# Kernel tuning notes

Hardware: AMD Instinct MI355X
Metric: run time of the kernel (lower is better)

Reference implementation:

```python
import jax, jax.numpy as jnp
import numpy as np

ATT_DIM = 1024
N_HEADS = 16
D_HEAD = ATT_DIM // N_HEADS
LARGE = 1e30  # fp32 masking constant used by masked_softmax


def setup_inputs() -> dict:
    key = jax.random.key(0)
    ks = jax.random.split(key, 12)
    B, Tq, Tv, D = 4, 2048, 2048, 1024
    s = 1.0 / np.sqrt(D)
    sf = 1.0 / np.sqrt(ATT_DIM)
    return {
        "query": jax.random.normal(ks[0], (B, Tq, D), jnp.float32),
        "value": jax.random.normal(ks[1], (B, Tv, D), jnp.float32),
        "value_lens": jax.random.randint(ks[2], (B,), 0, Tv, jnp.int32),
        "Wq": jax.random.normal(ks[3], (D, ATT_DIM), jnp.float32) * s,
        "bq": jnp.zeros((ATT_DIM,), jnp.float32),
        "Wk": jax.random.normal(ks[4], (D, ATT_DIM), jnp.float32) * s,
        "bk": jnp.zeros((ATT_DIM,), jnp.float32),
        "Wv": jax.random.normal(ks[5], (D, ATT_DIM), jnp.float32) * s,
        "bv": jnp.zeros((ATT_DIM,), jnp.float32),
        "Wf": jax.random.normal(ks[6], (ATT_DIM, ATT_DIM), jnp.float32) * sf,
        "bf": jnp.zeros((ATT_DIM,), jnp.float32),
    }


def _attention(query, value, value_lens, Wq, bq, Wk, bk, Wv, bv, Wf, bf):
    B, Tq, _ = query.shape
    Tv = value.shape[1]
    # projections
    k = value @ Wk + bk                     # [B,Tv,att_dim]
    v = value @ Wv + bv                     # [B,Tv,att_dim]
    q = (query @ Wq + bq) / jnp.sqrt(jnp.asarray(D_HEAD, query.dtype))
    # split heads
    q = q.reshape(B, Tq, N_HEADS, D_HEAD)
    k = k.reshape(B, Tv, N_HEADS, D_HEAD)
    v = v.reshape(B, Tv, N_HEADS, D_HEAD)
    # energy: [B, n_heads, Tq, Tv]
    energy = jnp.einsum("bind,bjnd->bnij", q, k)
    # sequence mask: [B,1,1,Tv]
    mask = (jnp.arange(Tv)[None, :] < value_lens[:, None]).astype(energy.dtype)
    energy = energy - (1.0 - mask)[:, None, None, :] * jnp.asarray(LARGE, energy.dtype)
    att_weight = jax.nn.softmax(energy, axis=-1)
    # context: [B, Tq, n_heads, d_head] -> [B, Tq, att_dim]
    context = jnp.einsum("bnij,bjnd->bind", att_weight, v).reshape(B, Tq, ATT_DIM)
    return context @ Wf + bf  # final_att (num_att_head > 1)


def reference(query, value, value_lens, Wq, bq, Wk, bk, Wv, bv, Wf, bf):
    return _attention(query, value, value_lens, Wq, bq, Wk, bk, Wv, bv, Wf, bf)
```

## Files before the change

### kernel.cpp

```cpp
#include <hip/hip_runtime.h>
#include <hip/hip_bf16.h>

typedef __attribute__((ext_vector_type(8))) short short8;
typedef __attribute__((ext_vector_type(4))) float f32x4;
typedef unsigned short u16;
typedef unsigned int u32;
typedef __attribute__((ext_vector_type(8))) unsigned short u16x8;
typedef __attribute__((ext_vector_type(4))) unsigned short u16x4;

__device__ __forceinline__ u16 f2bf(float f) {
    u32 u = __builtin_bit_cast(u32, f);
    u += 0x7FFFu + ((u >> 16) & 1u);
    return (u16)(u >> 16);
}
__device__ __forceinline__ u32 packbf2(float a, float b) {
    return ((u32)f2bf(b) << 16) | (u32)f2bf(a);
}
__device__ __forceinline__ float fexp2(float x) { return exp2f(x); }

__device__ __forceinline__ int swz(int row, int col) {
    return (row * 128 + col * 2) ^ ((row & 7) << 4);
}

__device__ __forceinline__ void gl16(const void* g, void* l) {
    __builtin_amdgcn_global_load_lds(
        (const __attribute__((address_space(1))) unsigned int*)g,
        (__attribute__((address_space(3))) unsigned int*)l, 16, 0, 0);
}

#define FENCE() asm volatile("" ::: "memory")
#define BARRIER() do { FENCE(); __builtin_amdgcn_s_barrier(); FENCE(); } while (0)

__global__ __launch_bounds__(256)
void cvt_kernel(const float* __restrict__ query, const float* __restrict__ value,
                u16* __restrict__ qB, u16* __restrict__ vB)
{
    int bid = blockIdx.x;
    const float* src; u16* dst;
    if (bid < 4096) { src = query; dst = qB; }
    else            { src = value; dst = vB; bid -= 4096; }
    const int i = bid * 256 + threadIdx.x;
    const float4 a = ((const float4*)src)[2 * i];
    const float4 b = ((const float4*)src)[2 * i + 1];
    u16x8 h;
    h[0] = f2bf(a.x); h[1] = f2bf(a.y); h[2] = f2bf(a.z); h[3] = f2bf(a.w);
    h[4] = f2bf(b.x); h[5] = f2bf(b.y); h[6] = f2bf(b.z); h[7] = f2bf(b.w);
    ((u16x8*)dst)[i] = h;
}

__global__ __launch_bounds__(256)
void wtrans_kernel(const float* __restrict__ W0, const float* __restrict__ W1,
                   const float* __restrict__ W2, const float* __restrict__ W3,
                   u16* __restrict__ T0, u16* __restrict__ T1,
                   u16* __restrict__ T2, u16* __restrict__ T3)
{
    const float* W; u16* T;
    switch (blockIdx.z) {
        case 0:  W = W0; T = T0; break;
        case 1:  W = W1; T = T1; break;
        case 2:  W = W2; T = T2; break;
        default: W = W3; T = T3; break;
    }
    __shared__ u16 tile[32][33];
    const int tid = threadIdx.x;
    const int n0 = blockIdx.x * 32, k0 = blockIdx.y * 32;
    const int r = tid >> 3, c = (tid & 7) * 4;
    float4 v = *(const float4*)(W + (size_t)(k0 + r) * 1024 + n0 + c);
    tile[c + 0][r] = f2bf(v.x);
    tile[c + 1][r] = f2bf(v.y);
    tile[c + 2][r] = f2bf(v.z);
    tile[c + 3][r] = f2bf(v.w);
    __syncthreads();
    u16x4 h;
    h[0] = tile[r][c]; h[1] = tile[r][c + 1]; h[2] = tile[r][c + 2]; h[3] = tile[r][c + 3];
    *(u16x4*)(T + (size_t)(n0 + r) * 1024 + k0 + c) = h;
}

#define GNK 32

__device__ __forceinline__ void stage_a(const u16* __restrict__ A, unsigned char* bufA,
                                        int row0, int kt, int tid) {
    const int r = tid >> 2, s = tid & 3;
    gl16((const unsigned char*)A + (size_t)(row0 + r) * 2048 + kt * 64 + ((s ^ (r & 3)) << 4),
         bufA + tid * 16);
}
__device__ __forceinline__ void stage_b(const u16* __restrict__ BT, unsigned char* bufB,
                                        int col0, int kt, int hb, int tid) {
    const int r = hb * 128 + (tid >> 2), s = tid & 3;
    gl16((const unsigned char*)BT + (size_t)(col0 + r) * 2048 + kt * 64 + ((s ^ (r & 3)) << 4),
         bufB + hb * 8192 + tid * 16);
}

__device__ __forceinline__ void gemm_core(const u16* __restrict__ A, const u16* __restrict__ BT,
                                          int row0, int col0, unsigned char* smem,
                                          int tid, int wm, int wn, int l15, int lhi,
                                          f32x4 acc[4][4])
{
    const int slot = (lhi ^ (l15 & 3)) << 4;
    #pragma unroll
    for (int kt = 0; kt < 3; ++kt) {
        unsigned char* buf = smem + kt * 24576;
        stage_a(A, buf, row0, kt, tid);
        stage_b(BT, buf + 8192, col0, kt, 0, tid);
        stage_b(BT, buf + 8192, col0, kt, 1, tid);
    }
    asm volatile("s_waitcnt vmcnt(6)" ::: "memory");
    BARRIER();

    for (int k = 0; k < GNK; ++k) {
        unsigned char* bufA = smem + (k & 3) * 24576;
        unsigned char* bufB = bufA + 8192;
        const bool st = (k + 3 < GNK);
        unsigned char* nbuf = smem + ((k + 3) & 3) * 24576;

        short8 a0, a1, a2, a3, b0, b1;
        a0 = *(const short8*)(bufA + (wm * 64 + 0 * 16 + l15) * 64 + slot);
        a1 = *(const short8*)(bufA + (wm * 64 + 1 * 16 + l15) * 64 + slot);
        a2 = *(const short8*)(bufA + (wm * 64 + 2 * 16 + l15) * 64 + slot);
        a3 = *(const short8*)(bufA + (wm * 64 + 3 * 16 + l15) * 64 + slot);
        b0 = *(const short8*)(bufB + (wn * 64 + 0 * 16 + l15) * 64 + slot);
        b1 = *(const short8*)(bufB + (wn * 64 + 1 * 16 + l15) * 64 + slot);
        if (st) stage_a(A, nbuf, row0, k + 3, tid);
        BARRIER();
        __builtin_amdgcn_s_setprio(1);
        acc[0][0] = __builtin_amdgcn_mfma_f32_16x16x32_bf16(a0, b0, acc[0][0], 0, 0, 0);
        acc[0][1] = __builtin_amdgcn_mfma_f32_16x16x32_bf16(a0, b1, acc[0][1], 0, 0, 0);
        acc[1][0] = __builtin_amdgcn_mfma_f32_16x16x32_bf16(a1, b0, acc[1][0], 0, 0, 0);
        acc[1][1] = __builtin_amdgcn_mfma_f32_16x16x32_bf16(a1, b1, acc[1][1], 0, 0, 0);
        acc[2][0] = __builtin_amdgcn_mfma_f32_16x16x32_bf16(a2, b0, acc[2][0], 0, 0, 0);
        acc[2][1] = __builtin_amdgcn_mfma_f32_16x16x32_bf16(a2, b1, acc[2][1], 0, 0, 0);
        acc[3][0] = __builtin_amdgcn_mfma_f32_16x16x32_bf16(a3, b0, acc[3][0], 0, 0, 0);
        acc[3][1] = __builtin_amdgcn_mfma_f32_16x16x32_bf16(a3, b1, acc[3][1], 0, 0, 0);
        __builtin_amdgcn_s_setprio(0);
        BARRIER();

        short8 b2, b3;
        b2 = *(const short8*)(bufB + (wn * 64 + 2 * 16 + l15) * 64 + slot);
        b3 = *(const short8*)(bufB + (wn * 64 + 3 * 16 + l15) * 64 + slot);
        if (st) {
            stage_b(BT, nbuf + 8192, col0, k + 3, 0, tid);
            stage_b(BT, nbuf + 8192, col0, k + 3, 1, tid);
        }
        if (k < GNK - 3)       asm volatile("s_waitcnt vmcnt(6)" ::: "memory");
        else if (k == GNK - 3) asm volatile("s_waitcnt vmcnt(3)" ::: "memory");
        else if (k == GNK - 2) asm volatile("s_waitcnt vmcnt(0)" ::: "memory");
        BARRIER();
        __builtin_amdgcn_s_setprio(1);
        acc[0][2] = __builtin_amdgcn_mfma_f32_16x16x32_bf16(a0, b2, acc[0][2], 0, 0, 0);
        acc[0][3] = __builtin_amdgcn_mfma_f32_16x16x32_bf16(a0, b3, acc[0][3], 0, 0, 0);
        acc[1][2] = __builtin_amdgcn_mfma_f32_16x16x32_bf16(a1, b2, acc[1][2], 0, 0, 0);
        acc[1][3] = __builtin_amdgcn_mfma_f32_16x16x32_bf16(a1, b3, acc[1][3], 0, 0, 0);
        acc[2][2] = __builtin_amdgcn_mfma_f32_16x16x32_bf16(a2, b2, acc[2][2], 0, 0, 0);
        acc[2][3] = __builtin_amdgcn_mfma_f32_16x16x32_bf16(a2, b3, acc[2][3], 0, 0, 0);
        acc[3][2] = __builtin_amdgcn_mfma_f32_16x16x32_bf16(a3, b2, acc[3][2], 0, 0, 0);
        acc[3][3] = __builtin_amdgcn_mfma_f32_16x16x32_bf16(a3, b3, acc[3][3], 0, 0, 0);
        __builtin_amdgcn_s_setprio(0);
        BARRIER();
    }
}

__global__ __launch_bounds__(512, 2)
void proj_kernel(const u16* __restrict__ queryB, const u16* __restrict__ valueB,
                 const u16* __restrict__ WqT, const u16* __restrict__ WkT,
                 const u16* __restrict__ WvT,
                 const float* __restrict__ bq, const float* __restrict__ bk,
                 const float* __restrict__ bv,
                 u16* __restrict__ Qb, u16* __restrict__ Kb, u16* __restrict__ Vt)
{
    __shared__ __align__(16) unsigned char smem[98304];
    const int t = (blockIdx.x & 7) * 96 + (blockIdx.x >> 3);
    const int z = t >> 8;
    const int tile = t & 255;
    const int row0 = (tile >> 2) * 128, col0 = (tile & 3) * 256;

    const u16* A    = (z == 0) ? queryB : valueB;
    const u16* BT   = (z == 0) ? WqT : (z == 1) ? WkT : WvT;
    const float* bias = (z == 0) ? bq : (z == 1) ? bk : bv;

    const int tid = threadIdx.x;
    const int lane = tid & 63, w = tid >> 6;
    const int wm = w >> 2, wn = w & 3;
    const int l15 = lane & 15, lhi = lane >> 4;

    f32x4 acc[4][4];
    const f32x4 fz = {0.f, 0.f, 0.f, 0.f};
    #pragma unroll
    for (int m = 0; m < 4; ++m)
        #pragma unroll
        for (int n = 0; n < 4; ++n) acc[m][n] = fz;

    gemm_core(A, BT, row0, col0, smem, tid, wm, wn, l15, lhi, acc);

    if (z < 2) {
        u16* out = (z == 0) ? Qb : Kb;
        const float scale = (z == 0) ? 0.18033688011112042f : 1.0f;
        const int bb = row0 >> 11;
        #pragma unroll
        for (int n = 0; n < 4; ++n) {
            int col = col0 + wn * 64 + n * 16 + l15;
            int hh = col >> 6, d = col & 63;
            float bv2 = bias[col];
            #pragma unroll
            for (int m = 0; m < 4; ++m) {
                int rbase = row0 + wm * 64 + m * 16 + lhi * 4;
                #pragma unroll
                for (int rr = 0; rr < 4; ++rr) {
                    int trow = (rbase + rr) & 2047;
                    out[(((size_t)bb * 16 + hh) * 2048 + trow) * 64 + d] =
                        f2bf((acc[m][n][rr] + bv2) * scale);
                }
            }
        }
    } else {
        __syncthreads();
        u16* vl = (u16*)smem;
        #pragma unroll
        for (int n = 0; n < 4; ++n) {
            int c = wn * 64 + n * 16 + l15;
            float bv2 = bias[col0 + c];
            #pragma unroll
            for (int m = 0; m < 4; ++m) {
                int rl = wm * 64 + m * 16 + lhi * 4;
                u16x4 h;
                #pragma unroll
                for (int rr = 0; rr < 4; ++rr) h[rr] = f2bf(acc[m][n][rr] + bv2);
                *(u16x4*)(vl + c * 132 + rl) = h;
            }
        }
        __syncthreads();
        const int bb = row0 >> 11, t0 = row0 & 2047;
        const int c = tid >> 1, hseg = tid & 1;
        const int col = col0 + c;
        const int hh = col >> 6, d = col & 63;
        size_t gb = (((size_t)bb * 16 + hh) * 64 + d) * 2048 + t0 + hseg * 64;
        #pragma unroll
        for (int j = 0; j < 8; ++j) {
            u16x8 v = *(const u16x8*)(vl + c * 132 + hseg * 64 + j * 8);
            *(u16x8*)(Vt + gb + j * 8) = v;
        }
    }
}

__global__ __launch_bounds__(512, 2)
void fgemm_kernel(const u16* __restrict__ Ctx, const u16* __restrict__ WfT,
                  const float* __restrict__ bias, float* __restrict__ out)
{
    __shared__ __align__(16) unsigned char smem[98304];
    const int t = (blockIdx.x & 7) * 32 + (blockIdx.x >> 3);
    const int row0 = (t >> 2) * 128, col0 = (t & 3) * 256;

    const int tid = threadIdx.x;
    const int lane = tid & 63, w = tid >> 6;
    const int wm = w >> 2, wn = w & 3;
    const int l15 = lane & 15, lhi = lane >> 4;

    f32x4 acc[4][4];
    const f32x4 fz = {0.f, 0.f, 0.f, 0.f};
    #pragma unroll
    for (int m = 0; m < 4; ++m)
        #pragma unroll
        for (int n = 0; n < 4; ++n) acc[m][n] = fz;

    gemm_core(Ctx, WfT, row0, col0, smem, tid, wm, wn, l15, lhi, acc);

    #pragma unroll
    for (int n = 0; n < 4; ++n) {
        int col = col0 + wn * 64 + n * 16 + l15;
        float bv2 = bias[col];
        #pragma unroll
        for (int m = 0; m < 4; ++m) {
            int rbase = row0 + wm * 64 + m * 16 + lhi * 4;
            #pragma unroll
            for (int rr = 0; rr < 4; ++rr)
                out[(size_t)(rbase + rr) * 1024 + col] = acc[m][n][rr] + bv2;
        }
    }
}

__global__ __launch_bounds__(512, 4)
void attn_kernel(const u16* __restrict__ Qb, const u16* __restrict__ Kb,
                 const u16* __restrict__ Vt, const int* __restrict__ lens,
                 u16* __restrict__ Ctx)
{
    __shared__ __align__(16) unsigned char ksm[2][8192];
    __shared__ __align__(16) unsigned char vsm[2][8192];

    const int tid = threadIdx.x;
    const int lane = tid & 63;
    const int w = tid >> 6;
    const int l15 = lane & 15, lhi = lane >> 4;
    const int t0id = (blockIdx.x & 7) * 128 + (blockIdx.x >> 3);
    const int qt = t0id & 15;
    const int hid2 = t0id >> 4;
    const int b = hid2 & 3, hh = hid2 >> 2;
    const size_t head = (size_t)(b * 16 + hh);
    const unsigned char* Kbase = (const unsigned char*)Kb + head * (2048 * 128);
    const unsigned char* Vbase = (const unsigned char*)Vt + head * (2048 * 128);
    const unsigned char* Qbase = (const unsigned char*)Qb + head * (2048 * 128) + (size_t)qt * (128 * 128);

    const int o0 = w * 1024 + lane * 16;
    const int r0 = o0 >> 7;
    const int sc0 = (o0 & 127) ^ ((r0 & 7) << 4);

    const int lens_b = lens[b];
    const bool uniform = (lens_b == 0);
    const int len = uniform ? 2048 : lens_b;
    const int nt = (len + 63) >> 6;
    const bool tail = (!uniform) && ((len & 63) != 0);

    auto stage = [&](int t, int bi) {
        gl16(Kbase + (size_t)t * 8192 + (size_t)r0 * 128 + sc0, ksm[bi] + o0);
        gl16(Vbase + (size_t)t * 128 + (size_t)r0 * 4096 + sc0, vsm[bi] + o0);
    };
    stage(0, 0);

    short8 qa[2];
    #pragma unroll
    for (int ks = 0; ks < 2; ++ks)
        qa[ks] = *(const short8*)(Qbase + (w * 16 + l15) * 128 + ks * 64 + lhi * 16);

    __syncthreads();

    float m = -1e30f, lsum = 0.f;
    const f32x4 fz = {0.f, 0.f, 0.f, 0.f};
    f32x4 cT[4];
    #pragma unroll
    for (int nf = 0; nf < 4; ++nf) cT[nf] = fz;

    const int srcA = l15 + (((2 * lhi) & 3) << 4);
    const int srcB = l15 + (((2 * lhi + 1) & 3) << 4);
    const bool hi = lhi >= 2;

    for (int t = 0; t < nt; ++t) {
        const int cur = t & 1;
        if (t + 1 < nt) stage(t + 1, cur ^ 1);

        f32x4 s[4];
        #pragma unroll
        for (int jf = 0; jf < 4; ++jf) s[jf] = fz;
        if (!uniform) {
            __builtin_amdgcn_s_setprio(1);
            #pragma unroll
            for (int ks = 0; ks < 2; ++ks)
                #pragma unroll
                for (int jf = 0; jf < 4; ++jf) {
                    short8 kb = *(const short8*)(ksm[cur] + swz(jf * 16 + l15, ks * 32 + lhi * 8));
                    s[jf] = __builtin_amdgcn_mfma_f32_16x16x32_bf16(kb, qa[ks], s[jf], 0, 0, 0);
                }
            __builtin_amdgcn_s_setprio(0);
            if (tail && t == nt - 1) {
                const int kvb = t * 64 + lhi * 4;
                #pragma unroll
                for (int jf = 0; jf < 4; ++jf)
                    #pragma unroll
                    for (int r = 0; r < 4; ++r)
                        if (kvb + jf * 16 + r >= len) s[jf][r] = -1e30f;
            }
        }
        f32x4 m4;
        #pragma unroll
        for (int r = 0; r < 4; ++r)
            m4[r] = fmaxf(fmaxf(s[0][r], s[1][r]), fmaxf(s[2][r], s[3][r]));
        float tmax = fmaxf(fmaxf(m4[0], m4[1]), fmaxf(m4[2], m4[3]));
        tmax = fmaxf(tmax, __shfl_xor(tmax, 16));
        tmax = fmaxf(tmax, __shfl_xor(tmax, 32));
        const float mnew = fmaxf(m, tmax);
        if (__any(tmax > m)) {
            const float sc = fexp2(m - mnew);
            lsum *= sc;
            #pragma unroll
            for (int nf = 0; nf < 4; ++nf)
                #pragma unroll
                for (int r = 0; r < 4; ++r) cT[nf][r] *= sc;
        }
        m = mnew;
        #pragma unroll
        for (int jf = 0; jf < 4; ++jf)
            #pragma unroll
            for (int r = 0; r < 4; ++r)
                s[jf][r] = fexp2(s[jf][r] - m);
        f32x4 s4;
        #pragma unroll
        for (int r = 0; r < 4; ++r)
            s4[r] = (s[0][r] + s[1][r]) + (s[2][r] + s[3][r]);
        float rs = (s4[0] + s4[1]) + (s4[2] + s4[3]);
        rs += __shfl_xor(rs, 16);
        rs += __shfl_xor(rs, 32);
        lsum += rs;
        u32 pk[4][2];
        #pragma unroll
        for (int jf = 0; jf < 4; ++jf) {
            pk[jf][0] = packbf2(s[jf][0], s[jf][1]);
            pk[jf][1] = packbf2(s[jf][2], s[jf][3]);
        }
        short8 pb[2];
        #pragma unroll
        for (int ks = 0; ks < 2; ++ks) {
            u32 a0, a1, a2, a3;
            { u32 x0 = (u32)__shfl((int)pk[2 * ks][0], srcA); u32 x1 = (u32)__shfl((int)pk[2 * ks + 1][0], srcA); a0 = hi ? x1 : x0; }
            { u32 x0 = (u32)__shfl((int)pk[2 * ks][1], srcA); u32 x1 = (u32)__shfl((int)pk[2 * ks + 1][1], srcA); a1 = hi ? x1 : x0; }
            { u32 x0 = (u32)__shfl((int)pk[2 * ks][0], srcB); u32 x1 = (u32)__shfl((int)pk[2 * ks + 1][0], srcB); a2 = hi ? x1 : x0; }
            { u32 x0 = (u32)__shfl((int)pk[2 * ks][1], srcB); u32 x1 = (u32)__shfl((int)pk[2 * ks + 1][1], srcB); a3 = hi ? x1 : x0; }
            typedef __attribute__((ext_vector_type(4))) unsigned int u32x4_t;
            u32x4_t av = {a0, a1, a2, a3};
            pb[ks] = __builtin_bit_cast(short8, av);
        }
        __builtin_amdgcn_s_setprio(1);
        #pragma unroll
        for (int ks = 0; ks < 2; ++ks)
            #pragma unroll
            for (int nf = 0; nf < 4; ++nf) {
                short8 vb = *(const short8*)(vsm[cur] + swz(nf * 16 + l15, ks * 32 + lhi * 8));
                cT[nf] = __builtin_amdgcn_mfma_f32_16x16x32_bf16(vb, pb[ks], cT[nf], 0, 0, 0);
            }
        __builtin_amdgcn_s_setprio(0);
        __syncthreads();
    }

    const float inv = 1.0f / lsum;
    const int trow = qt * 128 + w * 16 + l15;
    u16* op = Ctx + ((size_t)b * 2048 + trow) * 1024 + hh * 64 + lhi * 4;
    #pragma unroll
    for (int nf = 0; nf < 4; ++nf) {
        u16x4 h;
        #pragma unroll
        for (int r = 0; r < 4; ++r) h[r] = f2bf(cT[nf][r] * inv);
        *(u16x4*)(op + nf * 16) = h;
    }
}

extern "C" void kernel_launch(void* const* d_in, const int* in_sizes, int n_in,
                              void* d_out, int out_size, void* d_ws, size_t ws_size,
                              hipStream_t stream)
{
    (void)in_sizes; (void)n_in; (void)out_size; (void)ws_size;
    const float* query = (const float*)d_in[0];
    const float* value = (const float*)d_in[1];
    const int*   lens  = (const int*)d_in[2];
    const float* Wq = (const float*)d_in[3];
    const float* bq = (const float*)d_in[4];
    const float* Wk = (const float*)d_in[5];
    const float* bk = (const float*)d_in[6];
    const float* Wv = (const float*)d_in[7];
    const float* bv = (const float*)d_in[8];
    const float* Wf = (const float*)d_in[9];
    const float* bfp = (const float*)d_in[10];

    unsigned char* ws = (unsigned char*)d_ws;
    const size_t MB = (size_t)1 << 20;
    u16* WqT = (u16*)(ws + 0 * MB);
    u16* WkT = (u16*)(ws + 2 * MB);
    u16* WvT = (u16*)(ws + 4 * MB);
    u16* WfT = (u16*)(ws + 6 * MB);
    u16* Qb  = (u16*)(ws + 8 * MB);
    u16* Kb  = (u16*)(ws + 24 * MB);
    u16* Vt  = (u16*)(ws + 40 * MB);
    u16* Ctx = (u16*)(ws + 56 * MB);

    u16* queryB = (u16*)d_out;
    u16* valueB = queryB + (size_t)8192 * 1024;

    dim3 tb(256);
    cvt_kernel<<<dim3(8192), tb, 0, stream>>>(query, value, queryB, valueB);
    wtrans_kernel<<<dim3(32, 32, 4), tb, 0, stream>>>(Wq, Wk, Wv, Wf, WqT, WkT, WvT, WfT);

    proj_kernel<<<dim3(768), dim3(512), 0, stream>>>(queryB, valueB, WqT, WkT, WvT,
                                                     bq, bk, bv, Qb, Kb, Vt);

    attn_kernel<<<dim3(1024), dim3(512), 0, stream>>>(Qb, Kb, Vt, lens, Ctx);

    fgemm_kernel<<<dim3(256), dim3(512), 0, stream>>>(Ctx, WfT, bfp, (float*)d_out);
}
```

Baseline: 211.4 us.

## Compute softmax row sums via MFMA with ones, lazy rescale, hardware bf16 pack

The attention kernel drops the per-row sum of exponentials, which used a reduction tree plus cross-lane shuffles, and instead computes it with an extra MFMA that multiplies the bf16 probabilities by a ones vector. The running max is now updated only when the new max exceeds the old one by more than 8 (log2 domain), which skips most rescales of the accumulators. Manual bf16 rounding is replaced with the v_cvt_pk_bf16_f32 instruction. The trade-offs: the denominator is now summed from bf16-rounded probabilities, which matches the numerator's rounding, and the exponentials can grow up to 2^8 before a rescale, which costs some precision.

```diff
diff --git a/kernel.cpp b/kernel.cpp
--- a/kernel.cpp
+++ b/kernel.cpp
@@ -15,6 +15,11 @@
 }
 __device__ __forceinline__ u32 packbf2(float a, float b) {
     return ((u32)f2bf(b) << 16) | (u32)f2bf(a);
+}
+__device__ __forceinline__ u32 cvtpk(float a, float b) {
+    u32 r;
+    asm("v_cvt_pk_bf16_f32 %0, %1, %2" : "=v"(r) : "v"(a), "v"(b));
+    return r;
 }
 __device__ __forceinline__ float fexp2(float x) { return exp2f(x); }
 
@@ -319,10 +324,15 @@
     for (int ks = 0; ks < 2; ++ks)
         qa[ks] = *(const short8*)(Qbase + (w * 16 + l15) * 128 + ks * 64 + lhi * 16);
 
+    short8 onesv;
+    #pragma unroll
+    for (int i = 0; i < 8; ++i) onesv[i] = (short)0x3F80;
+
     __syncthreads();
 
-    float m = -1e30f, lsum = 0.f;
+    float m = -1e30f;
     const f32x4 fz = {0.f, 0.f, 0.f, 0.f};
+    f32x4 cs = fz;
     f32x4 cT[4];
     #pragma unroll
     for (int nf = 0; nf < 4; ++nf) cT[nf] = fz;
@@ -364,34 +374,27 @@
         float tmax = fmaxf(fmaxf(m4[0], m4[1]), fmaxf(m4[2], m4[3]));
         tmax = fmaxf(tmax, __shfl_xor(tmax, 16));
         tmax = fmaxf(tmax, __shfl_xor(tmax, 32));
-        const float mnew = fmaxf(m, tmax);
-        if (__any(tmax > m)) {
+        if (__any(tmax > m + 8.f)) {
+            const float mnew = fmaxf(m, tmax);
             const float sc = fexp2(m - mnew);
-            lsum *= sc;
+            #pragma unroll
+            for (int r = 0; r < 4; ++r) cs[r] *= sc;
             #pragma unroll
             for (int nf = 0; nf < 4; ++nf)
                 #pragma unroll
                 for (int r = 0; r < 4; ++r) cT[nf][r] *= sc;
-        }
-        m = mnew;
+            m = mnew;
+        }
         #pragma unroll
         for (int jf = 0; jf < 4; ++jf)
             #pragma unroll
             for (int r = 0; r < 4; ++r)
                 s[jf][r] = fexp2(s[jf][r] - m);
-        f32x4 s4;
-        #pragma unroll
-        for (int r = 0; r < 4; ++r)
-            s4[r] = (s[0][r] + s[1][r]) + (s[2][r] + s[3][r]);
-        float rs = (s4[0] + s4[1]) + (s4[2] + s4[3]);
-        rs += __shfl_xor(rs, 16);
-        rs += __shfl_xor(rs, 32);
-        lsum += rs;
         u32 pk[4][2];
         #pragma unroll
         for (int jf = 0; jf < 4; ++jf) {
-            pk[jf][0] = packbf2(s[jf][0], s[jf][1]);
-            pk[jf][1] = packbf2(s[jf][2], s[jf][3]);
+            pk[jf][0] = cvtpk(s[jf][0], s[jf][1]);
+            pk[jf][1] = cvtpk(s[jf][2], s[jf][3]);
         }
         short8 pb[2];
         #pragma unroll
@@ -407,17 +410,19 @@
         }
         __builtin_amdgcn_s_setprio(1);
         #pragma unroll
-        for (int ks = 0; ks < 2; ++ks)
+        for (int ks = 0; ks < 2; ++ks) {
+            cs = __builtin_amdgcn_mfma_f32_16x16x32_bf16(onesv, pb[ks], cs, 0, 0, 0);
             #pragma unroll
             for (int nf = 0; nf < 4; ++nf) {
                 short8 vb = *(const short8*)(vsm[cur] + swz(nf * 16 + l15, ks * 32 + lhi * 8));
                 cT[nf] = __builtin_amdgcn_mfma_f32_16x16x32_bf16(vb, pb[ks], cT[nf], 0, 0, 0);
             }
+        }
         __builtin_amdgcn_s_setprio(0);
         __syncthreads();
     }
 
-    const float inv = 1.0f / lsum;
+    const float inv = 1.0f / cs[0];
     const int trow = qt * 128 + w * 16 + l15;
     u16* op = Ctx + ((size_t)b * 2048 + trow) * 1024 + hh * 64 + lhi * 4;
     #pragma unroll
```

Measured after the change: 200.5 us. 1.05x faster.
